# Kernel optimization log

Hardware: AMD Instinct MI355X
Metric: run time of the kernel (lower is better)

The kernel has to match this reference:

```python
import jax, jax.numpy as jnp
import numpy as np

N = 50000      # nodes
K = 17         # regular degree (edges per node, pre-sorted by row)
D_IN = 128
D_OUT = 64
E = N * K


def setup_inputs() -> dict:
    key = jax.random.key(0)
    k1, k2, k3, k4, k5 = jax.random.split(key, 5)
    x = jax.random.normal(k1, (N, D_IN), dtype=jnp.float32)
    # edges sorted by row (required by dimmedian_idx); regular degree K
    row = jnp.repeat(jnp.arange(N, dtype=jnp.int32), K)
    col = jax.random.randint(k2, (E,), 0, N, dtype=jnp.int32)
    edge_index = jnp.stack([row, col], axis=0)
    edge_weight = jax.random.uniform(k3, (E,), dtype=jnp.float32)
    # glorot-style linear weight, zero-init-like small bias
    weight = jax.random.normal(k4, (D_IN, D_OUT), dtype=jnp.float32) * np.float32(1.0 / np.sqrt(D_IN))
    bias = jax.random.normal(k5, (D_OUT,), dtype=jnp.float32) * np.float32(0.01)
    return {"x": x, "edge_index": edge_index, "edge_weight": edge_weight,
            "weight": weight, "bias": bias}


def _weighted_dim_median(xp, col, w):
    """Per-node, per-dimension weighted median over neighbors (dimmedian_idx + gather).
    xp: [N, D] projected features; col: [E] neighbor ids; w: [E] edge weights.
    Exploits the regular degree K: edges for node i occupy rows i*K:(i+1)*K.
    """
    D = xp.shape[1]
    vals = xp[col].reshape(N, K, D)            # neighbor features per node
    wN = jnp.broadcast_to(w.reshape(N, K)[:, :, None], (N, K, D))
    order = jnp.argsort(vals, axis=1)          # sort neighbors per dim by value
    sorted_vals = jnp.take_along_axis(vals, order, axis=1)
    sorted_w = jnp.take_along_axis(wN, order, axis=1)
    cum = jnp.cumsum(sorted_w, axis=1)
    total = cum[:, -1:, :]
    # first sorted position where cumulative weight reaches half the total
    med_pos = jnp.argmax(cum >= 0.5 * total, axis=1)      # [N, D]
    med = jnp.take_along_axis(sorted_vals, med_pos[:, None, :], axis=1)[:, 0, :]
    return med


def reference(x, edge_index, edge_weight, weight, bias):
    xp = x @ weight                            # lin projection (no bias)
    row, col = edge_index[0], edge_index[1]
    med = _weighted_dim_median(xp, col, edge_weight)      # soft_median_reduce
    # row normalization: scatter_add of edge weights per destination row
    row_sum = jax.ops.segment_sum(edge_weight, row, num_segments=N)
    return row_sum[:, None] * med + bias
```

## Files before the change

### kernel.cpp

```cpp
#include <hip/hip_runtime.h>

#define N_NODES 50000
#define K_DEG   17
#define DIN     128
#define DOUT    64
#define KP      136

typedef __attribute__((ext_vector_type(8))) short  short8;
typedef __attribute__((ext_vector_type(4))) float  floatx4;

struct CEPair { unsigned char a, b; };

constexpr int net_count(int n) {
  int t = 0; while ((1 << t) < n) ++t;
  int cnt = 0;
  for (int p = 1 << (t - 1); p > 0; p >>= 1) {
    int q = 1 << (t - 1), r = 0, d = p;
    for (;;) {
      for (int i = 0; i < n - d; ++i)
        if ((i & p) == r) ++cnt;
      if (q == p) break;
      d = q - p; q >>= 1; r = p;
    }
  }
  return cnt;
}

template <int NP> struct NetArr { CEPair v[NP]; };

template <int NP>
constexpr NetArr<NP> net_pairs(int n) {
  NetArr<NP> out{};
  int t = 0; while ((1 << t) < n) ++t;
  int cnt = 0;
  for (int p = 1 << (t - 1); p > 0; p >>= 1) {
    int q = 1 << (t - 1), r = 0, d = p;
    for (;;) {
      for (int i = 0; i < n - d; ++i)
        if ((i & p) == r) {
          out.v[cnt].a = (unsigned char)i;
          out.v[cnt].b = (unsigned char)(i + d);
          ++cnt;
        }
      if (q == p) break;
      d = q - p; q >>= 1; r = p;
    }
  }
  return out;
}

constexpr int NP17 = net_count(K_DEG);

__device__ __forceinline__ unsigned int f2bf(float f) {
  union { float f; unsigned int u; } c; c.f = f;
  return (c.u + 0x7FFFu + ((c.u >> 16) & 1u)) >> 16;
}
__device__ __forceinline__ float bf2f(unsigned int b) {
  union { float f; unsigned int u; } c; c.u = b << 16;
  return c.f;
}

__global__ __launch_bounds__(256) void gemm_kernel(
    const float* __restrict__ x, const float* __restrict__ W,
    float* __restrict__ xp) {
  __shared__ unsigned short Wht[DOUT * KP];
  __shared__ unsigned short Wlt[DOUT * KP];

  const int t = threadIdx.x;

  {
    const float4* Wg4 = (const float4*)W;
    #pragma unroll
    for (int i = 0; i < 8; ++i) {
      int fi  = t + i * 256;
      int idx = fi * 4;
      int k   = idx >> 6;
      int n0  = idx & 63;
      float4 wv = Wg4[fi];
      float  f[4] = {wv.x, wv.y, wv.z, wv.w};
      #pragma unroll
      for (int e = 0; e < 4; ++e) {
        unsigned int hb = f2bf(f[e]);
        float        lo = f[e] - bf2f(hb);
        unsigned int lb = f2bf(lo);
        Wht[(n0 + e) * KP + k] = (unsigned short)hb;
        Wlt[(n0 + e) * KP + k] = (unsigned short)lb;
      }
    }
  }
  __syncthreads();

  const int wid   = t >> 6;
  const int lane  = t & 63;
  const int gwave = blockIdx.x * 4 + wid;
  if (gwave >= (N_NODES / 16)) return;

  const int r0 = gwave * 16;
  const int m  = lane & 15;
  const int q  = lane >> 4;

  const float4* x4 = (const float4*)x;
  float4 xr[8];
  #pragma unroll
  for (int ks = 0; ks < 4; ++ks) {
    int base = (r0 + m) * (DIN / 4) + ks * 8 + q * 2;
    xr[ks * 2 + 0] = x4[base + 0];
    xr[ks * 2 + 1] = x4[base + 1];
  }

  floatx4 acc[4];
  #pragma unroll
  for (int nt = 0; nt < 4; ++nt) acc[nt] = (floatx4){0.f, 0.f, 0.f, 0.f};

  const int nb = lane & 15;

  #pragma unroll
  for (int ks = 0; ks < 4; ++ks) {
    float f[8] = {xr[ks*2].x, xr[ks*2].y, xr[ks*2].z, xr[ks*2].w,
                  xr[ks*2+1].x, xr[ks*2+1].y, xr[ks*2+1].z, xr[ks*2+1].w};
    union { unsigned int i[4]; short8 s; } Ah, Al;
    #pragma unroll
    for (int r = 0; r < 4; ++r) {
      unsigned int h0 = f2bf(f[2*r]),   h1 = f2bf(f[2*r+1]);
      unsigned int l0 = f2bf(f[2*r]   - bf2f(h0));
      unsigned int l1 = f2bf(f[2*r+1] - bf2f(h1));
      Ah.i[r] = h0 | (h1 << 16);
      Al.i[r] = l0 | (l1 << 16);
    }
    const int kk = ks * 32 + q * 8;
    #pragma unroll
    for (int nt = 0; nt < 4; ++nt) {
      const int n = nt * 16 + nb;
      short8 Bh = *(const short8*)&Wht[n * KP + kk];
      short8 Bl = *(const short8*)&Wlt[n * KP + kk];
      acc[nt] = __builtin_amdgcn_mfma_f32_16x16x32_bf16(Al.s, Bh, acc[nt], 0, 0, 0);
      acc[nt] = __builtin_amdgcn_mfma_f32_16x16x32_bf16(Ah.s, Bl, acc[nt], 0, 0, 0);
      acc[nt] = __builtin_amdgcn_mfma_f32_16x16x32_bf16(Ah.s, Bh, acc[nt], 0, 0, 0);
    }
  }

  #pragma unroll
  for (int nt = 0; nt < 4; ++nt) {
    const int col = nt * 16 + nb;
    #pragma unroll
    for (int r = 0; r < 4; ++r) {
      const int row = r0 + q * 4 + r;
      xp[row * DOUT + col] = acc[nt][r];
    }
  }
}

__global__ __launch_bounds__(256) void median_kernel(
    const float* __restrict__ xp, const int* __restrict__ col,
    const float* __restrict__ ew, const float* __restrict__ bias,
    float* __restrict__ out) {
  const int wave = threadIdx.x >> 6;
  const int lane = threadIdx.x & 63;
  const int node = blockIdx.x * 4 + wave;
  if (node >= N_NODES) return;

  const int*   cp = col + node * K_DEG;
  const float* wp = ew  + node * K_DEG;

  float v[K_DEG], w[K_DEG];
  #pragma unroll
  for (int j = 0; j < K_DEG; ++j) {
    int c = cp[j];
    v[j] = xp[c * DOUT + lane];
    w[j] = wp[j];
  }

  float rs = 0.f;
  #pragma unroll
  for (int j = 0; j < K_DEG; ++j) rs += w[j];

  constexpr NetArr<NP17> NET = net_pairs<NP17>(K_DEG);
  #pragma unroll
  for (int s = 0; s < NP17; ++s) {
    const int a = NET.v[s].a, b = NET.v[s].b;
    float va = v[a], vb = v[b];
    bool sw = vb < va;
    float wa = w[a], wb = w[b];
    v[a] = sw ? vb : va;  v[b] = sw ? va : vb;
    w[a] = sw ? wb : wa;  w[b] = sw ? wa : wb;
  }

  float c[K_DEG];
  float run = 0.f;
  #pragma unroll
  for (int j = 0; j < K_DEG; ++j) { run += w[j]; c[j] = run; }
  const float half = 0.5f * run;

  float med = v[K_DEG - 1];
  #pragma unroll
  for (int j = K_DEG - 2; j >= 0; --j)
    med = (c[j] >= half) ? v[j] : med;

  out[node * DOUT + lane] = rs * med + bias[lane];
}

extern "C" void kernel_launch(void* const* d_in, const int* in_sizes, int n_in,
                              void* d_out, int out_size, void* d_ws, size_t ws_size,
                              hipStream_t stream) {
  const float* x    = (const float*)d_in[0];
  const int*   ei   = (const int*)d_in[1];
  const float* ew   = (const float*)d_in[2];
  const float* W    = (const float*)d_in[3];
  const float* bias = (const float*)d_in[4];
  float*       out  = (float*)d_out;
  float*       xp   = (float*)d_ws;
  const int*   colp = ei + (size_t)N_NODES * K_DEG;

  const int nwaves = N_NODES / 16;
  gemm_kernel<<<(nwaves + 3) / 4, 256, 0, stream>>>(x, W, xp);
  median_kernel<<<(N_NODES + 3) / 4, 256, 0, stream>>>(xp, colp, ew, bias, out);
}
```

Before: 131.3 us.

## Precompute split-bf16 weights in MFMA fragment layout via separate kernel

Adds a small pre-kernel that converts W once into hi/lo bf16 halves stored directly in the per-lane MFMA B-fragment order in workspace. The GEMM kernel then drops its per-block shared-memory staging, the conversion work and the __syncthreads, and loads B fragments as coalesced 16-byte global loads that should hit in cache. Each GEMM block previously re-converted the whole 128x64 weight matrix, so this removes redundant work and LDS pressure. In exchange it adds an extra kernel launch and relies on L2 caching for the repeated fragment loads.

```diff
diff --git a/kernel.cpp b/kernel.cpp
--- a/kernel.cpp
+++ b/kernel.cpp
@@ -4,7 +4,6 @@
 #define K_DEG   17
 #define DIN     128
 #define DOUT    64
-#define KP      136
 
 typedef __attribute__((ext_vector_type(8))) short  short8;
 typedef __attribute__((ext_vector_type(4))) float  floatx4;
@@ -60,41 +59,29 @@
   return c.f;
 }
 
+__global__ void convw_kernel(const float* __restrict__ W,
+                             unsigned short* __restrict__ T) {
+  const int flat = blockIdx.x * 256 + threadIdx.x;
+  const int j    = flat & 7;
+  const int lane = (flat >> 3) & 63;
+  const int pair = flat >> 9;
+  const int ks   = pair >> 2, nt = pair & 3;
+  const int k    = ks * 32 + (lane >> 4) * 8 + j;
+  const int n    = nt * 16 + (lane & 15);
+  const float f  = W[k * DOUT + n];
+  const unsigned int hb = f2bf(f);
+  const float        lo = f - bf2f(hb);
+  const unsigned int lb = f2bf(lo);
+  T[flat]        = (unsigned short)hb;
+  T[flat + 8192] = (unsigned short)lb;
+}
+
 __global__ __launch_bounds__(256) void gemm_kernel(
-    const float* __restrict__ x, const float* __restrict__ W,
+    const float* __restrict__ x, const unsigned short* __restrict__ T,
     float* __restrict__ xp) {
-  __shared__ unsigned short Wht[DOUT * KP];
-  __shared__ unsigned short Wlt[DOUT * KP];
-
-  const int t = threadIdx.x;
-
-  {
-    const float4* Wg4 = (const float4*)W;
-    #pragma unroll
-    for (int i = 0; i < 8; ++i) {
-      int fi  = t + i * 256;
-      int idx = fi * 4;
-      int k   = idx >> 6;
-      int n0  = idx & 63;
-      float4 wv = Wg4[fi];
-      float  f[4] = {wv.x, wv.y, wv.z, wv.w};
-      #pragma unroll
-      for (int e = 0; e < 4; ++e) {
-        unsigned int hb = f2bf(f[e]);
-        float        lo = f[e] - bf2f(hb);
-        unsigned int lb = f2bf(lo);
-        Wht[(n0 + e) * KP + k] = (unsigned short)hb;
-        Wlt[(n0 + e) * KP + k] = (unsigned short)lb;
-      }
-    }
-  }
-  __syncthreads();
-
-  const int wid   = t >> 6;
-  const int lane  = t & 63;
-  const int gwave = blockIdx.x * 4 + wid;
+  const int gwave = blockIdx.x * 4 + (threadIdx.x >> 6);
   if (gwave >= (N_NODES / 16)) return;
-
+  const int lane = threadIdx.x & 63;
   const int r0 = gwave * 16;
   const int m  = lane & 15;
   const int q  = lane >> 4;
@@ -103,7 +90,7 @@
   float4 xr[8];
   #pragma unroll
   for (int ks = 0; ks < 4; ++ks) {
-    int base = (r0 + m) * (DIN / 4) + ks * 8 + q * 2;
+    const int base = (r0 + m) * (DIN / 4) + ks * 8 + q * 2;
     xr[ks * 2 + 0] = x4[base + 0];
     xr[ks * 2 + 1] = x4[base + 1];
   }
@@ -112,41 +99,43 @@
   #pragma unroll
   for (int nt = 0; nt < 4; ++nt) acc[nt] = (floatx4){0.f, 0.f, 0.f, 0.f};
 
-  const int nb = lane & 15;
+  const short8* Th = (const short8*)T;
+  const short8* Tl = (const short8*)(T + 8192);
 
   #pragma unroll
   for (int ks = 0; ks < 4; ++ks) {
+    short8 Bh[4], Bl[4];
+    #pragma unroll
+    for (int nt = 0; nt < 4; ++nt) {
+      const int fi = (ks * 4 + nt) * 64 + lane;
+      Bh[nt] = Th[fi];
+      Bl[nt] = Tl[fi];
+    }
     float f[8] = {xr[ks*2].x, xr[ks*2].y, xr[ks*2].z, xr[ks*2].w,
                   xr[ks*2+1].x, xr[ks*2+1].y, xr[ks*2+1].z, xr[ks*2+1].w};
     union { unsigned int i[4]; short8 s; } Ah, Al;
     #pragma unroll
     for (int r = 0; r < 4; ++r) {
-      unsigned int h0 = f2bf(f[2*r]),   h1 = f2bf(f[2*r+1]);
-      unsigned int l0 = f2bf(f[2*r]   - bf2f(h0));
-      unsigned int l1 = f2bf(f[2*r+1] - bf2f(h1));
+      const unsigned int h0 = f2bf(f[2*r]),   h1 = f2bf(f[2*r+1]);
+      const unsigned int l0 = f2bf(f[2*r]   - bf2f(h0));
+      const unsigned int l1 = f2bf(f[2*r+1] - bf2f(h1));
       Ah.i[r] = h0 | (h1 << 16);
       Al.i[r] = l0 | (l1 << 16);
     }
-    const int kk = ks * 32 + q * 8;
     #pragma unroll
     for (int nt = 0; nt < 4; ++nt) {
-      const int n = nt * 16 + nb;
-      short8 Bh = *(const short8*)&Wht[n * KP + kk];
-      short8 Bl = *(const short8*)&Wlt[n * KP + kk];
-      acc[nt] = __builtin_amdgcn_mfma_f32_16x16x32_bf16(Al.s, Bh, acc[nt], 0, 0, 0);
-      acc[nt] = __builtin_amdgcn_mfma_f32_16x16x32_bf16(Ah.s, Bl, acc[nt], 0, 0, 0);
-      acc[nt] = __builtin_amdgcn_mfma_f32_16x16x32_bf16(Ah.s, Bh, acc[nt], 0, 0, 0);
+      acc[nt] = __builtin_amdgcn_mfma_f32_16x16x32_bf16(Al.s, Bh[nt], acc[nt], 0, 0, 0);
+      acc[nt] = __builtin_amdgcn_mfma_f32_16x16x32_bf16(Ah.s, Bl[nt], acc[nt], 0, 0, 0);
+      acc[nt] = __builtin_amdgcn_mfma_f32_16x16x32_bf16(Ah.s, Bh[nt], acc[nt], 0, 0, 0);
     }
   }
 
   #pragma unroll
   for (int nt = 0; nt < 4; ++nt) {
-    const int col = nt * 16 + nb;
-    #pragma unroll
-    for (int r = 0; r < 4; ++r) {
-      const int row = r0 + q * 4 + r;
-      xp[row * DOUT + col] = acc[nt][r];
-    }
+    const int col = nt * 16 + m;
+    #pragma unroll
+    for (int r = 0; r < 4; ++r)
+      xp[(r0 + q * 4 + r) * DOUT + col] = acc[nt][r];
   }
 }
 
@@ -208,10 +197,12 @@
   const float* W    = (const float*)d_in[3];
   const float* bias = (const float*)d_in[4];
   float*       out  = (float*)d_out;
-  float*       xp   = (float*)d_ws;
-  const int*   colp = ei + (size_t)N_NODES * K_DEG;
-
-  const int nwaves = N_NODES / 16;
-  gemm_kernel<<<(nwaves + 3) / 4, 256, 0, stream>>>(x, W, xp);
+
+  float*          xp = (float*)d_ws;
+  unsigned short* T  = (unsigned short*)((char*)d_ws + (size_t)N_NODES * DOUT * 4);
+  const int*      colp = ei + (size_t)N_NODES * K_DEG;
+
+  convw_kernel<<<8192 / 256, 256, 0, stream>>>(W, T);
+  gemm_kernel<<<(N_NODES / 16 + 3) / 4, 256, 0, stream>>>(x, T, xp);
   median_kernel<<<(N_NODES + 3) / 4, 256, 0, stream>>>(xp, colp, ew, bias, out);
 }
```

Measured after the change: 131.6 us. No clear change (+0.2%).
